# Optimization experiments

Measured on AMD Instinct MI355X. Metric: run time of the kernel, lower is better.

## Reference

```python
import jax, jax.numpy as jnp
import numpy as np
import math

BN_EPS = 1e-5
L2_EPS = 1e-12
TEMPARATURE = 0.01
Q_IN_DIM = 256


def _masked_bn(y, mask, gamma, beta):
    # y: [S, L, D], mask: [S, L] float (1 = valid packed row).
    # Emulates BatchNorm1d (training mode) over the packed valid rows.
    m = mask[..., None]
    cnt = jnp.sum(mask)
    mean = jnp.sum(y * m, axis=(0, 1)) / cnt
    var = jnp.sum(jnp.square(y - mean) * m, axis=(0, 1)) / cnt  # biased var
    return (y - mean) * jax.lax.rsqrt(var + BN_EPS) * gamma + beta


def _ctx_proj(x, W, b, gamma, beta, mask, normalize):
    y = jnp.einsum('sld,od->slo', x, W) + b
    y = jax.nn.relu(_masked_bn(y, mask, gamma, beta))
    if normalize:
        n = jnp.linalg.norm(y, axis=-1, keepdims=True)
        y = y / jnp.maximum(n, L2_EPS)
    return y


def setup_inputs() -> dict:
    key = jax.random.key(0)
    ks = jax.random.split(key, 8)
    S, La, Lb = 256, 128, 512
    Dq, Dkv, Dqk, Dv = 256, 265, 512, 512
    A = jax.random.normal(ks[0], (S, La, Dq), jnp.float32)
    B = jax.random.normal(ks[1], (S, Lb, Dkv), jnp.float32)
    a_lens = jax.random.randint(ks[2], (S,), 1, La + 1, jnp.int32)
    b_lens = jax.random.randint(ks[3], (S,), 1, Lb + 1, jnp.int32)
    pk = jax.random.split(ks[4], 4)
    sc = 0.05
    return {
        'A': A, 'B': B, 'a_lens': a_lens, 'b_lens': b_lens,
        'Wq': sc * jax.random.normal(pk[0], (Dqk, Dq), jnp.float32),
        'bq': jnp.zeros((Dqk,), jnp.float32),
        'gq': jnp.ones((Dqk,), jnp.float32),
        'betaq': jnp.zeros((Dqk,), jnp.float32),
        'Wk': sc * jax.random.normal(pk[1], (Dqk, Dkv), jnp.float32),
        'bk': jnp.zeros((Dqk,), jnp.float32),
        'gk': jnp.ones((Dqk,), jnp.float32),
        'betak': jnp.zeros((Dqk,), jnp.float32),
        'Wv': sc * jax.random.normal(pk[2], (Dv, Dkv), jnp.float32),
        'bv': jnp.zeros((Dv,), jnp.float32),
        'gv': jnp.ones((Dv,), jnp.float32),
        'betav': jnp.zeros((Dv,), jnp.float32),
        'Wf': sc * jax.random.normal(pk[3], (Dq, Dv), jnp.float32),
        'bf': jnp.zeros((Dq,), jnp.float32),
        'gf': jnp.ones((Dq,), jnp.float32),
        'betaf': jnp.zeros((Dq,), jnp.float32),
    }


def reference(A, B, a_lens, b_lens,
              Wq, bq, gq, betaq,
              Wk, bk, gk, betak,
              Wv, bv, gv, betav,
              Wf, bf, gf, betaf):
    S, La, _ = A.shape
    Lb = B.shape[1]
    mask_a = (jnp.arange(La)[None, :] < a_lens[:, None]).astype(A.dtype)  # [S, La]
    mask_b = (jnp.arange(Lb)[None, :] < b_lens[:, None]).astype(B.dtype)  # [S, Lb]

    q = _ctx_proj(A, Wq, bq, gq, betaq, mask_a, True)   # [S, La, Dqk]
    k = _ctx_proj(B, Wk, bk, gk, betak, mask_b, True)   # [S, Lb, Dqk]
    v = _ctx_proj(B, Wv, bv, gv, betav, mask_b, True)   # [S, Lb, Dv]

    scaler = 1.0 / (TEMPARATURE * math.sqrt(Q_IN_DIM))
    scores = jnp.einsum('sad,sbd->sab', q, k) * scaler  # [S, La, Lb]
    scores = jnp.where(mask_b[:, None, :] > 0, scores, -1e30)
    w = jax.nn.softmax(scores, axis=-1)
    wv = jnp.einsum('sab,sbd->sad', w, v)               # [S, La, Dv]

    f = _ctx_proj(wv, Wf, bf, gf, betaf, mask_a, False)  # [S, La, Dq]
    return f * mask_a[..., None]
```

## Files before the change

### kernel.cpp

```cpp
#include <hip/hip_runtime.h>
#include <hip/hip_bf16.h>
#include <stdint.h>


typedef __attribute__((ext_vector_type(8))) short short8;
typedef __attribute__((ext_vector_type(4))) float floatx4;

__device__ __forceinline__ float bf2f(short h) {
    union { unsigned u; float f; } c;
    c.u = ((unsigned)(unsigned short)h) << 16;
    return c.f;
}
__device__ __forceinline__ short f2bf(float f) {
    union { float f; unsigned u; } c;
    c.f = f;
    unsigned u = c.u + 0x7fffu + ((c.u >> 16) & 1u);
    return (short)(u >> 16);
}

__device__ __forceinline__ void async_cp16(const short* g, short* l) {
    __builtin_amdgcn_global_load_lds(
        (const __attribute__((address_space(1))) unsigned int*)g,
        (__attribute__((address_space(3))) unsigned int*)l, 16, 0, 0);
}

__device__ __forceinline__ short8 cvt8load(const float* p) {
    float4 f0 = *(const float4*)(p);
    float4 f1 = *(const float4*)(p + 4);
    short8 r;
    r[0] = f2bf(f0.x); r[1] = f2bf(f0.y); r[2] = f2bf(f0.z); r[3] = f2bf(f0.w);
    r[4] = f2bf(f1.x); r[5] = f2bf(f1.y); r[6] = f2bf(f1.z); r[7] = f2bf(f1.w);
    return r;
}
__device__ __forceinline__ short8 cvt8guard(const float* row, int c0, int Kin) {
    short8 r;
#pragma unroll
    for (int j = 0; j < 8; j++) {
        int c = c0 + j;
        r[j] = (c < Kin) ? f2bf(row[c]) : (short)0;
    }
    return r;
}

__global__ __launch_bounds__(256) void cvt_pad(const float* __restrict__ in,
                                               short* __restrict__ out,
                                               int kin, int kout) {
    long row = blockIdx.x;
    const float* src = in + row * (long)kin;
    short* dst = out + row * (long)kout;
    for (int c = threadIdx.x; c < kout; c += 256)
        dst[c] = (c < kin) ? f2bf(src[c]) : (short)0;
}

__global__ __launch_bounds__(256, 3)
void gemm128(const short* __restrict__ X,
             const short* __restrict__ W0, const short* __restrict__ W1,
             const float* __restrict__ bias0, const float* __restrict__ bias1,
             short* __restrict__ Y0, short* __restrict__ Y1,
             float* __restrict__ st0, float* __restrict__ st1,
             int N, int Kp, const int* __restrict__ lens, int Lshift,
             int nShift, int dual)
{
    __shared__ short SH[16384];
    const int lin = blockIdx.x;
    const int xcd = lin & 7, sl = lin >> 3;
    const int nb = sl & ((1 << nShift) - 1);
    const int ms = sl >> nShift;
    const int m0 = (ms * 8 + xcd) * 128;
    int g = 0, n0;
    if (dual) { g = nb & 1; n0 = (nb >> 1) * 128; } else { n0 = nb * 128; }
    const short* W    = g ? W1 : W0;
    const float* bias = g ? bias1 : bias0;
    short* Y          = g ? Y1 : Y0;
    float* stats      = g ? st1 : st0;

    const int tid = threadIdx.x;
    const int l = tid & 63, w = tid >> 6;
    const int quad = l >> 4, l15 = l & 15;
    const int wr = w & 1, wc = w >> 1;
    const int mo = wr * 64, no = wc * 64;

    floatx4 acc[4][4];
#pragma unroll
    for (int i = 0; i < 4; i++)
#pragma unroll
        for (int j = 0; j < 4; j++) acc[i][j] = (floatx4){0.f, 0.f, 0.f, 0.f};

    const int srow = tid >> 2;
    const int scol = (tid & 3) * 8;
    const short* Xs = X + (long)(m0 + srow) * Kp + scol;
    const short* Ws = W + (long)(n0 + srow) * Kp + scol;
    const long strideR = (long)64 * Kp;
    const int nsteps = Kp >> 5;

    {
        short* At = SH;
        short* Bt = SH + 4096;
#pragma unroll
        for (int c = 0; c < 2; c++)
            async_cp16(Xs + c * strideR, At + c * 2048 + tid * 8);
#pragma unroll
        for (int c = 0; c < 2; c++)
            async_cp16(Ws + c * strideR, Bt + c * 2048 + tid * 8);
    }
    __syncthreads();

    int cur = 0;
    for (int t = 0; t < nsteps; t++) {
        if (t + 1 < nsteps) {
            short* At = SH + (cur ^ 1) * 8192;
            short* Bt = At + 4096;
            const short* Xk = Xs + (t + 1) * 32;
            const short* Wk = Ws + (t + 1) * 32;
#pragma unroll
            for (int c = 0; c < 2; c++)
                async_cp16(Xk + c * strideR, At + c * 2048 + tid * 8);
#pragma unroll
            for (int c = 0; c < 2; c++)
                async_cp16(Wk + c * strideR, Bt + c * 2048 + tid * 8);
        }
        const short* At = SH + cur * 8192;
        const short* Bt = At + 4096;
        short8 af[4], bfr[4];
#pragma unroll
        for (int i = 0; i < 4; i++)
            af[i] = *(const short8*)(At + (mo + i * 16 + l15) * 32 + quad * 8);
#pragma unroll
        for (int j = 0; j < 4; j++)
            bfr[j] = *(const short8*)(Bt + (no + j * 16 + l15) * 32 + quad * 8);
#pragma unroll
        for (int i = 0; i < 4; i++)
#pragma unroll
            for (int j = 0; j < 4; j++)
                acc[i][j] = __builtin_amdgcn_mfma_f32_16x16x32_bf16(af[i], bfr[j], acc[i][j], 0, 0, 0);
        __syncthreads();
        cur ^= 1;
    }

    const int Lmask = (1 << Lshift) - 1;
    float msk[4][4];
#pragma unroll
    for (int i = 0; i < 4; i++)
#pragma unroll
        for (int r = 0; r < 4; r++) {
            int rg = m0 + mo + i * 16 + quad * 4 + r;
            msk[i][r] = ((rg & Lmask) < lens[rg >> Lshift]) ? 1.f : 0.f;
        }
    float bv[4];
#pragma unroll
    for (int j = 0; j < 4; j++) bv[j] = bias[n0 + no + j * 16 + l15];

#pragma unroll
    for (int j = 0; j < 4; j++) {
        float ps = 0.f, pss = 0.f;
#pragma unroll
        for (int i = 0; i < 4; i++)
#pragma unroll
            for (int r = 0; r < 4; r++) {
                float v = acc[i][j][r] + bv[j];
                ps += v * msk[i][r];
                pss += v * v * msk[i][r];
            }
        ps  += __shfl_xor(ps, 16, 64);  ps  += __shfl_xor(ps, 32, 64);
        pss += __shfl_xor(pss, 16, 64); pss += __shfl_xor(pss, 32, 64);
        if (l < 16) {
            atomicAdd(&stats[n0 + no + j * 16 + l15], ps);
            atomicAdd(&stats[N + n0 + no + j * 16 + l15], pss);
        }
    }

    short* Cs = SH;
#pragma unroll
    for (int pass = 0; pass < 2; pass++) {
        __syncthreads();
        if (wr == pass) {
#pragma unroll
            for (int j = 0; j < 4; j++)
#pragma unroll
                for (int i = 0; i < 4; i++)
#pragma unroll
                    for (int r = 0; r < 4; r++)
                        Cs[(i * 16 + quad * 4 + r) * 132 + no + j * 16 + l15] =
                            f2bf(acc[i][j][r] + bv[j]);
        }
        __syncthreads();
#pragma unroll
        for (int c = 0; c < 4; c++) {
            int e = c * 2048 + tid * 8;
            int row = e >> 7, col = e & 127;
            short8 vv = *(const short8*)(Cs + row * 132 + col);
            *(short8*)(Y + (long)(m0 + pass * 64 + row) * N + n0 + col) = vv;
        }
    }
}

template<bool XBF16, bool KAL>
__global__ __launch_bounds__(256, 2)
void gemm_bt(const void* __restrict__ Xp, const float* __restrict__ W,
             const float* __restrict__ bias, short* __restrict__ Y,
             int N, int Kin, int Kp, float* __restrict__ stats,
             const int* __restrict__ lens, int Lshift)
{
    __shared__ short At[128 * 32];
    __shared__ short Bt[128 * 32];
    const int m0 = blockIdx.x * 128;
    const int n0 = blockIdx.y * 128;
    const int tid = threadIdx.x;
    const int w = tid >> 6, l = tid & 63;
    const int quad = l >> 4, l15 = l & 15;
    const int mo = (w & 1) * 64, no = (w >> 1) * 64;

    floatx4 acc[4][4];
#pragma unroll
    for (int i = 0; i < 4; i++)
#pragma unroll
        for (int j = 0; j < 4; j++) acc[i][j] = (floatx4){0.f, 0.f, 0.f, 0.f};

    const int srow = tid >> 2;
    const int sc8 = (tid & 3) * 8;

    for (int k0 = 0; k0 < Kp; k0 += 32) {
        __syncthreads();
        const int c0 = k0 + sc8;
        short8 a0, a1, b0, b1;
        if (XBF16) {
            const short* X = (const short*)Xp;
            a0 = *(const short8*)(X + (long)(m0 + srow) * Kp + c0);
            a1 = *(const short8*)(X + (long)(m0 + 64 + srow) * Kp + c0);
        } else {
            const float* X = (const float*)Xp;
            if (KAL) {
                a0 = cvt8load(X + (long)(m0 + srow) * Kin + c0);
                a1 = cvt8load(X + (long)(m0 + 64 + srow) * Kin + c0);
            } else {
                a0 = cvt8guard(X + (long)(m0 + srow) * Kin, c0, Kin);
                a1 = cvt8guard(X + (long)(m0 + 64 + srow) * Kin, c0, Kin);
            }
        }
        if (KAL) {
            b0 = cvt8load(W + (long)(n0 + srow) * Kin + c0);
            b1 = cvt8load(W + (long)(n0 + 64 + srow) * Kin + c0);
        } else {
            b0 = cvt8guard(W + (long)(n0 + srow) * Kin, c0, Kin);
            b1 = cvt8guard(W + (long)(n0 + 64 + srow) * Kin, c0, Kin);
        }
        *(short8*)(At + srow * 32 + sc8) = a0;
        *(short8*)(At + (64 + srow) * 32 + sc8) = a1;
        *(short8*)(Bt + srow * 32 + sc8) = b0;
        *(short8*)(Bt + (64 + srow) * 32 + sc8) = b1;
        __syncthreads();
        short8 af[4], bfr[4];
#pragma unroll
        for (int i = 0; i < 4; i++) {
            af[i]  = *(const short8*)(At + (mo + i * 16 + l15) * 32 + quad * 8);
            bfr[i] = *(const short8*)(Bt + (no + i * 16 + l15) * 32 + quad * 8);
        }
#pragma unroll
        for (int i = 0; i < 4; i++)
#pragma unroll
            for (int j = 0; j < 4; j++)
                acc[i][j] = __builtin_amdgcn_mfma_f32_16x16x32_bf16(af[i], bfr[j], acc[i][j], 0, 0, 0);
    }

    const int Lmask = (1 << Lshift) - 1;
    float msk[4][4];
#pragma unroll
    for (int i = 0; i < 4; i++)
#pragma unroll
        for (int r = 0; r < 4; r++) {
            int rg = m0 + mo + i * 16 + quad * 4 + r;
            msk[i][r] = ((rg & Lmask) < lens[rg >> Lshift]) ? 1.f : 0.f;
        }
#pragma unroll
    for (int j = 0; j < 4; j++) {
        int colj = n0 + no + j * 16 + l15;
        float bvs = bias[colj];
        float ps = 0.f, pss = 0.f;
#pragma unroll
        for (int i = 0; i < 4; i++)
#pragma unroll
            for (int r = 0; r < 4; r++) {
                int rg = m0 + mo + i * 16 + quad * 4 + r;
                float v = acc[i][j][r] + bvs;
                Y[(long)rg * N + colj] = f2bf(v);
                ps += v * msk[i][r];
                pss += v * v * msk[i][r];
            }
        ps  += __shfl_xor(ps, 16, 64);  ps  += __shfl_xor(ps, 32, 64);
        pss += __shfl_xor(pss, 16, 64); pss += __shfl_xor(pss, 32, 64);
        if (l < 16) {
            atomicAdd(&stats[colj], ps);
            atomicAdd(&stats[N + colj], pss);
        }
    }
}

__global__ void finalize_stats(float* __restrict__ stats, const float* __restrict__ g,
                               const float* __restrict__ beta,
                               const int* __restrict__ lens, int C)
{
    __shared__ int lred[256];
    int t = threadIdx.x;
    if (t < 256) lred[t] = lens[t];
    __syncthreads();
    for (int s2 = 128; s2 > 0; s2 >>= 1) {
        if (t < s2) lred[t] += lred[t + s2];
        __syncthreads();
    }
    float cnt = (float)lred[0];
    if (t < C) {
        float mean = stats[t] / cnt;
        float var = fmaxf(stats[C + t] / cnt - mean * mean, 0.f);
        float a = rsqrtf(var + 1e-5f) * g[t];
        stats[t] = a;
        stats[C + t] = beta[t] - mean * a;
    }
}

__global__ __launch_bounds__(256)
void apply_norm512(short* __restrict__ Y, const float* __restrict__ stats)
{
    int w = threadIdx.x >> 6, l = threadIdx.x & 63;
    long row = (long)blockIdx.x * 4 + w;
    short8 yv = *(const short8*)(Y + row * 512 + l * 8);
    float v[8];
    float ss = 0.f;
#pragma unroll
    for (int i = 0; i < 8; i++) {
        int c = l * 8 + i;
        float t = fmaxf(bf2f(yv[i]) * stats[c] + stats[512 + c], 0.f);
        v[i] = t;
        ss += t * t;
    }
#pragma unroll
    for (int off = 1; off < 64; off <<= 1) ss += __shfl_xor(ss, off, 64);
    float scl = 1.f / fmaxf(sqrtf(ss), 1e-12f);
    short8 o;
#pragma unroll
    for (int i = 0; i < 8; i++) o[i] = f2bf(v[i] * scl);
    *(short8*)(Y + row * 512 + l * 8) = o;
}

__global__ __launch_bounds__(256)
void attention(const short* __restrict__ q, const short* __restrict__ k,
               const short* __restrict__ v, const int* __restrict__ b_lens,
               short* __restrict__ wv, int wvStride)
{
    __shared__ short tile[32 * 520];
    __shared__ short Pscr[4][16 * 40];
    const int lin = blockIdx.x;
    const int xcd = lin & 7, sl = lin >> 3;
    const int a0 = (sl & 1) * 64;
    const int s = (sl >> 1) * 8 + xcd;
    const int tid = threadIdx.x;
    const int w = tid >> 6, l = tid & 63;
    const int quad = l >> 4, l15 = l & 15;
    const int blen = b_lens[s];
    const int sr = tid >> 3;
    const int scg = (tid & 7) * 8;

    short8 qf[16];
    const short* qbase = q + ((long)(s * 128 + a0 + w * 16 + l15)) * 512 + quad * 8;
#pragma unroll
    for (int kk = 0; kk < 16; kk++) qf[kk] = *(const short8*)(qbase + kk * 32);

    floatx4 sc[32];
#pragma unroll
    for (int i = 0; i < 32; i++) sc[i] = (floatx4){0.f, 0.f, 0.f, 0.f};

    const short* kbase = k + (long)s * 512 * 512;
    for (int bt2 = 0; bt2 < 16; ++bt2) {
        __syncthreads();
        const short* krow = kbase + (long)(bt2 * 32 + sr) * 512;
#pragma unroll
        for (int i = 0; i < 2; i++) {
            short8 t0 = *(const short8*)(krow + i * 256 + scg);
            short8 t1 = *(const short8*)(krow + i * 256 + 64 + scg);
            short8 t2 = *(const short8*)(krow + i * 256 + 128 + scg);
            short8 t3 = *(const short8*)(krow + i * 256 + 192 + scg);
            *(short8*)(&tile[sr * 520 + i * 256 + scg]) = t0;
            *(short8*)(&tile[sr * 520 + i * 256 + 64 + scg]) = t1;
            *(short8*)(&tile[sr * 520 + i * 256 + 128 + scg]) = t2;
            *(short8*)(&tile[sr * 520 + i * 256 + 192 + scg]) = t3;
        }
        __syncthreads();
#pragma unroll
        for (int kk = 0; kk < 16; kk++) {
            short8 f0 = *(const short8*)(&tile[l15 * 520 + kk * 32 + quad * 8]);
            short8 f1 = *(const short8*)(&tile[(16 + l15) * 520 + kk * 32 + quad * 8]);
            sc[bt2 * 2]     = __builtin_amdgcn_mfma_f32_16x16x32_bf16(qf[kk], f0, sc[bt2 * 2], 0, 0, 0);
            sc[bt2 * 2 + 1] = __builtin_amdgcn_mfma_f32_16x16x32_bf16(qf[kk], f1, sc[bt2 * 2 + 1], 0, 0, 0);
        }
    }

    const float scaler = 6.25f;
    float mrow[4] = {-__builtin_inff(), -__builtin_inff(), -__builtin_inff(), -__builtin_inff()};
#pragma unroll
    for (int bt = 0; bt < 32; ++bt) {
        bool valid = (bt * 16 + l15) < blen;
#pragma unroll
        for (int r = 0; r < 4; r++) {
            float v2 = valid ? sc[bt][r] * scaler : -__builtin_inff();
            sc[bt][r] = v2;
            mrow[r] = fmaxf(mrow[r], v2);
        }
    }
#pragma unroll
    for (int r = 0; r < 4; r++) {
#pragma unroll
        for (int off = 1; off < 16; off <<= 1)
            mrow[r] = fmaxf(mrow[r], __shfl_xor(mrow[r], off, 64));
    }
    float ssum[4] = {0.f, 0.f, 0.f, 0.f};
#pragma unroll
    for (int bt = 0; bt < 32; ++bt)
#pragma unroll
        for (int r = 0; r < 4; r++) {
            float p = __expf(sc[bt][r] - mrow[r]);
            sc[bt][r] = p;
            ssum[r] += p;
        }
#pragma unroll
    for (int r = 0; r < 4; r++) {
#pragma unroll
        for (int off = 1; off < 16; off <<= 1) ssum[r] += __shfl_xor(ssum[r], off, 64);
        ssum[r] = 1.f / ssum[r];
    }

    short8 pf[16];
    short* Pw = Pscr[w];
#pragma unroll
    for (int kk = 0; kk < 16; kk++) {
#pragma unroll
        for (int half = 0; half < 2; half++)
#pragma unroll
            for (int r = 0; r < 4; r++)
                Pw[(quad * 4 + r) * 40 + half * 16 + l15] = f2bf(sc[kk * 2 + half][r] * ssum[r]);
        pf[kk] = *(const short8*)(&Pw[l15 * 40 + quad * 8]);
    }

    const short* vbase = v + (long)s * 512 * 512;
    short* wvbase = wv + (long)(s * 128 + a0 + w * 16 + quad * 4) * wvStride;
    for (int dt = 0; dt < 16; ++dt) {
        __syncthreads();
#pragma unroll
        for (int round = 0; round < 2; round++) {
            int b = round * 256 + tid;
            const short* vr = vbase + (long)b * 512 + dt * 32;
            short8 x0 = *(const short8*)(vr);
            short8 x1 = *(const short8*)(vr + 8);
            short8 x2 = *(const short8*)(vr + 16);
            short8 x3 = *(const short8*)(vr + 24);
#pragma unroll
            for (int j = 0; j < 8; j++) {
                tile[j * 520 + b]        = x0[j];
                tile[(8 + j) * 520 + b]  = x1[j];
                tile[(16 + j) * 520 + b] = x2[j];
                tile[(24 + j) * 520 + b] = x3[j];
            }
        }
        __syncthreads();
        floatx4 o0 = (floatx4){0.f, 0.f, 0.f, 0.f};
        floatx4 o1 = (floatx4){0.f, 0.f, 0.f, 0.f};
#pragma unroll
        for (int kk = 0; kk < 16; kk++) {
            short8 f0 = *(const short8*)(&tile[l15 * 520 + kk * 32 + quad * 8]);
            short8 f1 = *(const short8*)(&tile[(16 + l15) * 520 + kk * 32 + quad * 8]);
            o0 = __builtin_amdgcn_mfma_f32_16x16x32_bf16(pf[kk], f0, o0, 0, 0, 0);
            o1 = __builtin_amdgcn_mfma_f32_16x16x32_bf16(pf[kk], f1, o1, 0, 0, 0);
        }
#pragma unroll
        for (int r = 0; r < 4; r++) {
            wvbase[(long)r * wvStride + dt * 32 + l15]      = f2bf(o0[r]);
            wvbase[(long)r * wvStride + dt * 32 + 16 + l15] = f2bf(o1[r]);
        }
    }

    if (wvStride > 512) {
        int r = tid >> 2, cb = (tid & 3) * 16;
        short8 z = (short8){0, 0, 0, 0, 0, 0, 0, 0};
        short* pz = wv + (long)(s * 128 + a0 + r) * wvStride + 512 + cb;
        *(short8*)(pz) = z;
        *(short8*)(pz + 8) = z;
    }
}

__global__ __launch_bounds__(256)
void apply_f(const short* __restrict__ Yf, const float* __restrict__ stats,
             const int* __restrict__ a_lens, float* __restrict__ out)
{
    const long total = (long)32768 * 256;
    for (long e = (long)blockIdx.x * 256 + threadIdx.x; e < total; e += (long)gridDim.x * 256) {
        int c = (int)(e & 255);
        long row = e >> 8;
        int sI = (int)(row >> 7), pos = (int)(row & 127);
        float v = fmaxf(bf2f(Yf[e]) * stats[c] + stats[256 + c], 0.f);
        out[e] = (pos < a_lens[sI]) ? v : 0.f;
    }
}

extern "C" void kernel_launch(void* const* d_in, const int* in_sizes, int n_in,
                              void* d_out, int out_size, void* d_ws, size_t ws_size,
                              hipStream_t stream)
{
    (void)in_sizes; (void)n_in; (void)out_size;
    const float* A     = (const float*)d_in[0];
    const float* B     = (const float*)d_in[1];
    const int* a_lens  = (const int*)d_in[2];
    const int* b_lens  = (const int*)d_in[3];
    const float* Wq    = (const float*)d_in[4];
    const float* bq    = (const float*)d_in[5];
    const float* gq    = (const float*)d_in[6];
    const float* betaq = (const float*)d_in[7];
    const float* Wk    = (const float*)d_in[8];
    const float* bk    = (const float*)d_in[9];
    const float* gk    = (const float*)d_in[10];
    const float* betak = (const float*)d_in[11];
    const float* Wv    = (const float*)d_in[12];
    const float* bv    = (const float*)d_in[13];
    const float* gv    = (const float*)d_in[14];
    const float* betav = (const float*)d_in[15];
    const float* Wf    = (const float*)d_in[16];
    const float* bfp   = (const float*)d_in[17];
    const float* gf    = (const float*)d_in[18];
    const float* betaf = (const float*)d_in[19];
    float* out = (float*)d_out;
    char* base = (char*)d_ws;

    const size_t oWqb = 0;
    const size_t oWkb = oWqb + 294912;
    const size_t oWvb = oWkb + 294912;
    const size_t oWfb = oWvb + 294912;
    const size_t oBbf = oWfb + 294912;
    const size_t oQb  = oBbf + 75497472;
    const size_t oYv  = oQb + 33554432;
    const size_t oKb  = oYv + 134217728;
    const size_t oSt  = oKb + 134217728;
    const size_t FAST_NEED = oSt + 16384;

    if (ws_size >= FAST_NEED) {
        short* Wqb = (short*)(base + oWqb);
        short* Wkb = (short*)(base + oWkb);
        short* Wvb = (short*)(base + oWvb);
        short* Wfb = (short*)(base + oWfb);
        short* Bbf = (short*)(base + oBbf);
        short* qb  = (short*)(base + oQb);
        short* Yv  = (short*)(base + oYv);
        short* kb  = (short*)(base + oKb);
        short* Abf = (short*)(base + oKb);
        short* wvb = (short*)(base + oBbf);
        short* Yf  = (short*)(base + oQb);
        float* stQ = (float*)(base + oSt);
        float* stK = stQ + 1024;
        float* stV = stQ + 2048;
        float* stF = stQ + 3072;

        hipMemsetAsync(stQ, 0, 16384, stream);

        cvt_pad<<<32768, 256, 0, stream>>>(A, Abf, 256, 288);
        cvt_pad<<<131072, 256, 0, stream>>>(B, Bbf, 265, 288);
        cvt_pad<<<512, 256, 0, stream>>>(Wq, Wqb, 256, 288);
        cvt_pad<<<512, 256, 0, stream>>>(Wk, Wkb, 265, 288);
        cvt_pad<<<512, 256, 0, stream>>>(Wv, Wvb, 265, 288);
        cvt_pad<<<256, 256, 0, stream>>>(Wf, Wfb, 512, 576);

        gemm128<<<1024, 256, 0, stream>>>(
            Abf, Wqb, Wqb, bq, bq, qb, qb, stQ, stQ, 512, 288, a_lens, 7, 2, 0);
        gemm128<<<8192, 256, 0, stream>>>(
            Bbf, Wvb, Wkb, bv, bk, Yv, kb, stV, stK, 512, 288, b_lens, 9, 3, 1);

        finalize_stats<<<1, 512, 0, stream>>>(stV, gv, betav, b_lens, 512);
        finalize_stats<<<1, 512, 0, stream>>>(stK, gk, betak, b_lens, 512);
        finalize_stats<<<1, 512, 0, stream>>>(stQ, gq, betaq, a_lens, 512);
        apply_norm512<<<32768, 256, 0, stream>>>(Yv, stV);
        apply_norm512<<<32768, 256, 0, stream>>>(kb, stK);
        apply_norm512<<<8192, 256, 0, stream>>>(qb, stQ);

        attention<<<512, 256, 0, stream>>>(qb, kb, Yv, b_lens, wvb, 576);

        gemm128<<<512, 256, 0, stream>>>(
            wvb, Wfb, Wfb, bfp, bfp, Yf, Yf, stF, stF, 256, 576, a_lens, 7, 1, 0);
        finalize_stats<<<1, 512, 0, stream>>>(stF, gf, betaf, a_lens, 256);
        apply_f<<<8192, 256, 0, stream>>>(Yf, stF, a_lens, out);
        return;
    }

    short* qb  = (short*)(base);
    short* Yv  = (short*)(base + 33554432);
    short* kb  = (short*)(base + 33554432 + 134217728);
    short* wvb = (short*)(base + 33554432 + 2L * 134217728);
    float* stQ = (float*)(base + 2L * 33554432 + 2L * 134217728);
    float* stK = stQ + 1024;
    float* stV = stQ + 2048;
    float* stF = stQ + 3072;
    short* Yf  = qb;

    hipMemsetAsync(stQ, 0, 16384, stream);

    gemm_bt<false, true><<<dim3(256, 4), 256, 0, stream>>>(
        A, Wq, bq, qb, 512, 256, 256, stQ, a_lens, 7);
    gemm_bt<false, false><<<dim3(1024, 4), 256, 0, stream>>>(
        B, Wv, bv, Yv, 512, 265, 288, stV, b_lens, 9);
    finalize_stats<<<1, 512, 0, stream>>>(stV, gv, betav, b_lens, 512);
    apply_norm512<<<32768, 256, 0, stream>>>(Yv, stV);
    gemm_bt<false, false><<<dim3(1024, 4), 256, 0, stream>>>(
        B, Wk, bk, kb, 512, 265, 288, stK, b_lens, 9);
    finalize_stats<<<1, 512, 0, stream>>>(stK, gk, betak, b_lens, 512);
    apply_norm512<<<32768, 256, 0, stream>>>(kb, stK);
    finalize_stats<<<1, 512, 0, stream>>>(stQ, gq, betaq, a_lens, 512);
    apply_norm512<<<8192, 256, 0, stream>>>(qb, stQ);
    attention<<<512, 256, 0, stream>>>(qb, kb, Yv, b_lens, wvb, 512);
    gemm_bt<true, true><<<dim3(256, 2), 256, 0, stream>>>(
        wvb, Wf, bfp, Yf, 256, 512, 512, stF, a_lens, 7);
    finalize_stats<<<1, 512, 0, stream>>>(stF, gf, betaf, a_lens, 256);
    apply_f<<<8192, 256, 0, stream>>>(Yf, stF, a_lens, out);
}
```

Measured before the change: 851.3 us.

## Triple-buffer gemm128 LDS tiles with explicit vmcnt-based waits

The projection GEMM moves from double to triple buffering of its LDS tiles. Prefetch now runs two K-steps ahead, and the full __syncthreads is replaced by a counted s_waitcnt vmcnt plus a raw s_barrier, so loads for later steps can stay in flight while the current step computes. This targets global-memory latency that the single-step prefetch left exposed. The cost is 48KB of LDS per block instead of 32KB, which could limit occupancy, and the hand-counted vmcnt values depend on each stage issuing exactly four loads.

```diff
diff --git a/kernel.cpp b/kernel.cpp
--- a/kernel.cpp
+++ b/kernel.cpp
@@ -61,7 +61,7 @@
              int N, int Kp, const int* __restrict__ lens, int Lshift,
              int nShift, int dual)
 {
-    __shared__ short SH[16384];
+    __shared__ short SH[24576];
     const int lin = blockIdx.x;
     const int xcd = lin & 7, sl = lin >> 3;
     const int nb = sl & ((1 << nShift) - 1);
@@ -93,32 +93,29 @@
     const long strideR = (long)64 * Kp;
     const int nsteps = Kp >> 5;
 
-    {
-        short* At = SH;
-        short* Bt = SH + 4096;
-#pragma unroll
-        for (int c = 0; c < 2; c++)
-            async_cp16(Xs + c * strideR, At + c * 2048 + tid * 8);
-#pragma unroll
-        for (int c = 0; c < 2; c++)
-            async_cp16(Ws + c * strideR, Bt + c * 2048 + tid * 8);
-    }
-    __syncthreads();
+    auto stage = [&](int buf, int t) {
+        short* At = SH + buf * 8192;
+        short* Bt = At + 4096;
+        const short* Xk = Xs + t * 32;
+        const short* Wk = Ws + t * 32;
+        async_cp16(Xk,           At + tid * 8);
+        async_cp16(Xk + strideR, At + 2048 + tid * 8);
+        async_cp16(Wk,           Bt + tid * 8);
+        async_cp16(Wk + strideR, Bt + 2048 + tid * 8);
+    };
+
+    stage(0, 0);
+    if (nsteps > 1) stage(1, 1);
+    if (nsteps > 2) stage(2, 2);
 
     int cur = 0;
     for (int t = 0; t < nsteps; t++) {
-        if (t + 1 < nsteps) {
-            short* At = SH + (cur ^ 1) * 8192;
-            short* Bt = At + 4096;
-            const short* Xk = Xs + (t + 1) * 32;
-            const short* Wk = Ws + (t + 1) * 32;
-#pragma unroll
-            for (int c = 0; c < 2; c++)
-                async_cp16(Xk + c * strideR, At + c * 2048 + tid * 8);
-#pragma unroll
-            for (int c = 0; c < 2; c++)
-                async_cp16(Wk + c * strideR, Bt + c * 2048 + tid * 8);
-        }
+        if (t + 2 < nsteps)      asm volatile("s_waitcnt vmcnt(8)" ::: "memory");
+        else if (t + 1 < nsteps) asm volatile("s_waitcnt vmcnt(4)" ::: "memory");
+        else                     asm volatile("s_waitcnt vmcnt(0)" ::: "memory");
+        __builtin_amdgcn_s_barrier();
+        __builtin_amdgcn_sched_barrier(0);
+
         const short* At = SH + cur * 8192;
         const short* Bt = At + 4096;
         short8 af[4], bfr[4];
@@ -133,8 +130,11 @@
 #pragma unroll
             for (int j = 0; j < 4; j++)
                 acc[i][j] = __builtin_amdgcn_mfma_f32_16x16x32_bf16(af[i], bfr[j], acc[i][j], 0, 0, 0);
-        __syncthreads();
-        cur ^= 1;
+
+        __builtin_amdgcn_sched_barrier(0);
+        __builtin_amdgcn_s_barrier();
+        if (t + 3 < nsteps) stage(cur, t + 3);
+        cur = (cur == 2) ? 0 : cur + 1;
     }
 
     const int Lmask = (1 << Lshift) - 1;
```

After: 837.2 us. Within noise of the previous version (-1.7%).
